# Kernel optimization log

Measured on AMD Instinct MI355X. Metric: run time of the kernel, lower is better.

The kernel has to match this reference:

```python
import jax, jax.numpy as jnp
import numpy as np

B, D, H, T = 4096, 256, 266, 51   # batch, dim, dim+10 hidden, timegrid points
S = T - 1                          # Euler steps
KAPPA, SIGMA = 1.0, 1.0
EPS = 1e-5                         # BatchNorm eps (torch default)


def setup_inputs() -> dict:
    key = jax.random.key(0)
    ks = iter(jax.random.split(key, 16))

    def lin(nin, nout, prefix=()):
        return jax.random.normal(next(ks), prefix + (nin, nout), jnp.float32) / np.float32(np.sqrt(nin))

    inp = {}
    inp["x"] = jax.random.normal(next(ks), (B, D), jnp.float32)
    # per-timestep stacks: Linear+BN params for i_h1, h1_h2, and Linear for h2_o
    inp["W1"] = lin(D, H, (S,));  inp["b1"] = jnp.zeros((S, H));  inp["g1"] = jnp.ones((S, H));  inp["be1"] = jnp.zeros((S, H))
    inp["W2"] = lin(H, H, (S,));  inp["b2"] = jnp.zeros((S, H));  inp["g2"] = jnp.ones((S, H));  inp["be2"] = jnp.zeros((S, H))
    inp["W3"] = lin(H, D, (S,));  inp["b3"] = jnp.zeros((S, D))
    # v0 head: three hiddenLayers (Linear+BN+ReLU), last one width 1
    inp["vW1"] = lin(D, H);  inp["vb1"] = jnp.zeros((H,));  inp["vg1"] = jnp.ones((H,));  inp["vbe1"] = jnp.zeros((H,))
    inp["vW2"] = lin(H, H);  inp["vb2"] = jnp.zeros((H,));  inp["vg2"] = jnp.ones((H,));  inp["vbe2"] = jnp.zeros((H,))
    inp["vW3"] = lin(H, 1);  inp["vb3"] = jnp.zeros((1,));  inp["vg3"] = jnp.ones((1,));  inp["vbe3"] = jnp.zeros((1,))
    # frozen external netAlpha: (dim+1) -> H -> dim MLP
    inp["aW1"] = lin(D + 1, H);  inp["ab1"] = jnp.zeros((H,))
    inp["aW2"] = lin(H, D);      inp["ab2"] = jnp.zeros((D,))
    # law (population mean per step), timegrid, Brownian increments xi
    inp["law"] = jax.random.normal(next(ks), (S, D), jnp.float32) * 0.1
    inp["timegrid"] = jnp.linspace(0.0, 1.0, T, dtype=jnp.float32)
    inp["xi"] = jax.random.normal(next(ks), (S, B, D), jnp.float32)
    return inp


def _bn(h, g, b):
    # BatchNorm1d in training mode: batch stats (biased variance), affine
    mu = h.mean(axis=0)
    var = h.var(axis=0)
    return g * (h - mu) / jnp.sqrt(var + EPS) + b


def _hid(h, W, b, g, be):
    return jax.nn.relu(_bn(h @ W + b, g, be))


def reference(x, W1, b1, g1, be1, W2, b2, g2, be2, W3, b3,
              vW1, vb1, vg1, vbe1, vW2, vb2, vg2, vbe2, vW3, vb3, vg3, vbe3,
              aW1, ab1, aW2, ab2, law, timegrid, xi):
    x0 = x
    # v0 head evaluated on initial x (i == 0 branch)
    v0 = _hid(x0, vW1, vb1, vg1, vbe1)
    v0 = _hid(v0, vW2, vb2, vg2, vbe2)
    v0 = _hid(v0, vW3, vb3, vg3, vbe3)            # [B, 1]

    hs = jnp.diff(timegrid)                        # [S]
    ts = timegrid[:-1]                             # [S]

    def step(carry, inp):
        xc, vc = carry
        (W1i, b1i, g1i, be1i, W2i, b2i, g2i, be2i, W3i, b3i, lawi, ti, hi, xii) = inp
        h1 = _hid(xc, W1i, b1i, g1i, be1i)
        h2 = _hid(h1, W2i, b2i, g2i, be2i)
        grad = h2 @ W3i + b3i                      # [B, D]
        tx = jnp.concatenate([jnp.full((xc.shape[0], 1), ti, xc.dtype), xc], axis=1)
        alpha = jax.nn.relu(tx @ aW1 + ab1) @ aW2 + ab2   # [B, D]
        f = 0.5 * KAPPA * jnp.sum((xc - lawi) ** 2, axis=1) + 0.5 * jnp.sum(alpha ** 2, axis=1)
        sq = SIGMA * jnp.sqrt(hi)
        # diag(grad @ (sigma*sqrt(h)*xi).T) == row-wise dot product
        ito = sq * jnp.sum(grad * xii, axis=1)     # [B]
        vn = vc - (f * hi)[:, None] + ito[:, None]
        xn = xc + alpha * hi + sq * xii
        return (xn, vn), xn

    (xf, v), xs = jax.lax.scan(
        step, (x0, v0),
        (W1, b1, g1, be1, W2, b2, g2, be2, W3, b3, law, ts, hs, xi))
    path = jnp.concatenate([x0[None], xs], axis=0)  # [T, B, D]
    return (v, xf, path)
```

## Files before the change

### kernel.cpp

```cpp
#include <hip/hip_runtime.h>
#include <math.h>

#define B_   4096
#define D_   256
#define H_   266
#define T_   51
#define S_   50
#define HP   320
#define EPSF 1e-5f

typedef __bf16 bf16_t;
typedef __bf16 bf16x8 __attribute__((ext_vector_type(8)));
typedef float  f32x4  __attribute__((ext_vector_type(4)));

#define BM 64
#define BN 64
#define BK 64
#define LDST 72

struct Job {
  const float* A; int lda; int Ka;
  const float* g; const float* be;
  const float* asum; const float* asq;
  int bnA;
  const bf16_t* Wt; int ldw;
  const float* bias;
  const float* trow; const float* tg; int tidx;
  float* C; int ldc; int N; int relu;
  float* ssum; float* ssq;
  int mode;
  const float* xc; const float* xi; const float* law;
  float* xn; float* vacc;
};

__device__ __forceinline__ void load16(const float* p, float* a) {
  const float4* q = (const float4*)p;
  float4 v0 = q[0], v1 = q[1], v2 = q[2], v3 = q[3];
  a[0]=v0.x; a[1]=v0.y; a[2]=v0.z;  a[3]=v0.w;
  a[4]=v1.x; a[5]=v1.y; a[6]=v1.z;  a[7]=v1.w;
  a[8]=v2.x; a[9]=v2.y; a[10]=v2.z; a[11]=v2.w;
  a[12]=v3.x; a[13]=v3.y; a[14]=v3.z; a[15]=v3.w;
}

__global__ __launch_bounds__(256) void mfma_gemm(Job j0, Job j1, Job j2, float invB) {
  Job j = (blockIdx.z == 0) ? j0 : ((blockIdx.z == 1) ? j1 : j2);

  const int r0 = blockIdx.y * BM;
  const int c0 = blockIdx.x * BN;
  if (c0 >= j.N) return;

  __shared__ bf16_t As[BM][LDST];
  __shared__ bf16_t Ws[BN][LDST];
  __shared__ float sc[HP], sh[HP];

  const int tid = threadIdx.x;

  if (j.bnA) {
    for (int k = tid; k < HP; k += 256) {
      if (k < j.Ka) {
        float mu  = j.asum[k] * invB;
        float var = j.asq[k] * invB - mu * mu;
        float s   = j.g[k] * rsqrtf(var + EPSF);
        sc[k] = s; sh[k] = j.be[k] - mu * s;
      } else { sc[k] = 0.f; sh[k] = 0.f; }
    }
  }

  const int wave = tid >> 6;
  const int lane = tid & 63;
  const int wr = (wave >> 1) * 32;
  const int wc = (wave & 1) * 32;
  const int l16 = lane & 15;
  const int lk8 = (lane >> 4) * 8;

  f32x4 acc[2][2] = {};

  const int arow = tid >> 2;
  const int kseg = (tid & 3) * 16;

  const int niter = (j.Ka + BK - 1) / BK;

  const float*  Abase = j.A + (size_t)(r0 + arow) * j.lda + kseg;
  const int     crow  = c0 + arow;
  const bf16_t* Wbase = j.Wt + (size_t)crow * j.ldw + kseg;
  const bool    wok   = crow < j.N;

  float a16[16];
  uint4 wv0 = make_uint4(0,0,0,0), wv1 = make_uint4(0,0,0,0);

  load16(Abase, a16);
  if (wok) {
    const uint4* q = (const uint4*)Wbase;
    wv0 = q[0]; wv1 = q[1];
  }

  for (int it = 0; it < niter; ++it) {
    const int kb = it * BK + kseg;

    __syncthreads();

    bf16x8 p0, p1;
    if (j.bnA) {
      #pragma unroll
      for (int i = 0; i < 8; ++i)
        p0[i] = (bf16_t)fmaxf(fmaf(a16[i], sc[kb + i], sh[kb + i]), 0.f);
      #pragma unroll
      for (int i = 0; i < 8; ++i)
        p1[i] = (bf16_t)fmaxf(fmaf(a16[8 + i], sc[kb + 8 + i], sh[kb + 8 + i]), 0.f);
    } else {
      #pragma unroll
      for (int i = 0; i < 8; ++i) {
        float t = (kb + i < j.Ka) ? a16[i] : 0.f;
        p0[i] = (bf16_t)t;
      }
      #pragma unroll
      for (int i = 0; i < 8; ++i) {
        float t = (kb + 8 + i < j.Ka) ? a16[8 + i] : 0.f;
        p1[i] = (bf16_t)t;
      }
    }
    *(bf16x8*)&As[arow][kseg]     = p0;
    *(bf16x8*)&As[arow][kseg + 8] = p1;
    *(uint4*)&Ws[arow][kseg]      = wv0;
    *(uint4*)&Ws[arow][kseg + 8]  = wv1;

    __syncthreads();

    if (it + 1 < niter) {
      load16(Abase + (size_t)(it + 1) * BK, a16);
      if (wok) {
        const uint4* q = (const uint4*)(Wbase + (size_t)(it + 1) * BK);
        wv0 = q[0]; wv1 = q[1];
      }
    }

    bf16x8 af[2][2], bfr[2][2];
    #pragma unroll
    for (int mi = 0; mi < 2; ++mi)
      #pragma unroll
      for (int kk = 0; kk < 2; ++kk)
        af[mi][kk] = *(const bf16x8*)&As[wr + mi*16 + l16][kk*32 + lk8];
    #pragma unroll
    for (int ni = 0; ni < 2; ++ni)
      #pragma unroll
      for (int kk = 0; kk < 2; ++kk)
        bfr[ni][kk] = *(const bf16x8*)&Ws[wc + ni*16 + l16][kk*32 + lk8];
    #pragma unroll
    for (int kk = 0; kk < 2; ++kk)
      #pragma unroll
      for (int mi = 0; mi < 2; ++mi)
        #pragma unroll
        for (int ni = 0; ni < 2; ++ni)
          acc[mi][ni] = __builtin_amdgcn_mfma_f32_16x16x32_bf16(af[mi][kk], bfr[ni][kk], acc[mi][ni], 0, 0, 0);
  }

  float tb = j.trow ? j.tg[j.tidx] : 0.f;
  float vv[2][2][4];
  #pragma unroll
  for (int ni = 0; ni < 2; ++ni) {
    int col = c0 + wc + ni*16 + l16;
    bool cok = col < j.N;
    float bias = cok ? j.bias[col] : 0.f;
    if (j.trow && cok) bias = fmaf(tb, j.trow[col], bias);
    #pragma unroll
    for (int mi = 0; mi < 2; ++mi)
      #pragma unroll
      for (int r = 0; r < 4; ++r) {
        float v = acc[mi][ni][r] + bias;
        if (j.relu) v = fmaxf(v, 0.f);
        vv[mi][ni][r] = v;
      }
  }

  if (j.mode == 0) {
    #pragma unroll
    for (int ni = 0; ni < 2; ++ni) {
      int col = c0 + wc + ni*16 + l16;
      bool cok = col < j.N;
      float s = 0.f, q = 0.f;
      #pragma unroll
      for (int mi = 0; mi < 2; ++mi)
        #pragma unroll
        for (int r = 0; r < 4; ++r) {
          float v = vv[mi][ni][r];
          int row = r0 + wr + mi*16 + ((lane >> 4) << 2) + r;
          if (cok) j.C[(size_t)row * j.ldc + col] = v;
          s += v; q += v * v;
        }
      if (j.ssum) {
        s += __shfl_xor(s, 16); q += __shfl_xor(q, 16);
        s += __shfl_xor(s, 32); q += __shfl_xor(q, 32);
        if (lane < 16) {
          int col2 = c0 + wc + ni*16 + lane;
          if (col2 < j.N) { atomicAdd(&j.ssum[col2], s); atomicAdd(&j.ssq[col2], q); }
        }
      }
    }
  } else {
    float hi = j.tg[j.tidx + 1] - j.tg[j.tidx];
    float sq = sqrtf(hi);
    #pragma unroll
    for (int mi = 0; mi < 2; ++mi) {
      #pragma unroll
      for (int r = 0; r < 4; ++r) {
        int row = r0 + wr + mi*16 + ((lane >> 4) << 2) + r;
        float part = 0.f;
        #pragma unroll
        for (int ni = 0; ni < 2; ++ni) {
          int col = c0 + wc + ni*16 + l16;
          size_t off = (size_t)row * D_ + col;
          float v = vv[mi][ni][r];
          if (j.mode == 1) {
            float xcv = j.xc[off];
            float xiv = j.xi[off];
            float lw  = j.law[col];
            j.xn[off] = xcv + v * hi + sq * xiv;
            float df = xcv - lw;
            part += df * df + v * v;
          } else {
            part += v * j.xi[off];
          }
        }
        part += __shfl_xor(part, 1); part += __shfl_xor(part, 2);
        part += __shfl_xor(part, 4); part += __shfl_xor(part, 8);
        if (l16 == 0)
          atomicAdd(&j.vacc[row], (j.mode == 1) ? -0.5f * hi * part : sq * part);
      }
    }
  }
}

__global__ __launch_bounds__(256) void wconv(const float* __restrict__ in, bf16_t* __restrict__ out,
                                             int K, int N, int Kp, int total) {
  for (int idx = blockIdx.x * 256 + threadIdx.x; idx < total; idx += gridDim.x * 256) {
    int k = idx % Kp; int rest = idx / Kp; int n = rest % N; int s = rest / N;
    float v = (k < K) ? in[((size_t)s * K + k) * N + n] : 0.f;
    out[idx] = (bf16_t)v;
  }
}

__global__ __launch_bounds__(256) void matvec_bn(const float* __restrict__ A, int lda,
                                                 const float* __restrict__ g, const float* __restrict__ be,
                                                 const float* __restrict__ asum, const float* __restrict__ asq,
                                                 const float* __restrict__ w, const float* __restrict__ bptr,
                                                 float* __restrict__ y, float* ssum, float* ssq,
                                                 int K, float invB) {
  int r = blockIdx.x;
  float acc = 0.f;
  for (int k = threadIdx.x; k < K; k += 256) {
    float mu  = asum[k] * invB;
    float var = asq[k] * invB - mu * mu;
    float s   = g[k] * rsqrtf(var + EPSF);
    float val = fmaxf(fmaf(A[(size_t)r * lda + k], s, be[k] - mu * s), 0.f);
    acc += val * w[k];
  }
  __shared__ float sred[256];
  sred[threadIdx.x] = acc; __syncthreads();
  for (int st = 128; st > 0; st >>= 1) {
    if (threadIdx.x < st) sred[threadIdx.x] += sred[threadIdx.x + st];
    __syncthreads();
  }
  if (threadIdx.x == 0) {
    float v = sred[0] + bptr[0];
    y[r] = v;
    atomicAdd(ssum, v); atomicAdd(ssq, v * v);
  }
}

__global__ __launch_bounds__(256) void v0_fin(const float* __restrict__ y, float* v,
                                              const float* g, const float* be,
                                              const float* ssum, const float* ssq,
                                              int M, float invM) {
  int r = blockIdx.x * blockDim.x + threadIdx.x;
  if (r < M) {
    float mu  = ssum[0] * invM;
    float var = ssq[0] * invM - mu * mu;
    float t = g[0] * (y[r] - mu) * rsqrtf(var + EPSF) + be[0];
    v[r] = fmaxf(t, 0.f);
  }
}

__global__ __launch_bounds__(256) void vadd(float* __restrict__ v, const float* __restrict__ vacc, int M) {
  int r = blockIdx.x * 256 + threadIdx.x;
  if (r < M) v[r] += vacc[r];
}

extern "C" void kernel_launch(void* const* d_in, const int* in_sizes, int n_in,
                              void* d_out, int out_size, void* d_ws, size_t ws_size,
                              hipStream_t stream) {
  const float* x    = (const float*)d_in[0];
  const float* W1   = (const float*)d_in[1];
  const float* b1   = (const float*)d_in[2];
  const float* g1   = (const float*)d_in[3];
  const float* be1  = (const float*)d_in[4];
  const float* W2   = (const float*)d_in[5];
  const float* b2   = (const float*)d_in[6];
  const float* g2   = (const float*)d_in[7];
  const float* be2  = (const float*)d_in[8];
  const float* W3   = (const float*)d_in[9];
  const float* b3   = (const float*)d_in[10];
  const float* vW1  = (const float*)d_in[11];
  const float* vb1  = (const float*)d_in[12];
  const float* vg1  = (const float*)d_in[13];
  const float* vbe1 = (const float*)d_in[14];
  const float* vW2  = (const float*)d_in[15];
  const float* vb2  = (const float*)d_in[16];
  const float* vg2  = (const float*)d_in[17];
  const float* vbe2 = (const float*)d_in[18];
  const float* vW3  = (const float*)d_in[19];
  const float* vb3  = (const float*)d_in[20];
  const float* vg3  = (const float*)d_in[21];
  const float* vbe3 = (const float*)d_in[22];
  const float* aW1  = (const float*)d_in[23];
  const float* ab1  = (const float*)d_in[24];
  const float* aW2  = (const float*)d_in[25];
  const float* ab2  = (const float*)d_in[26];
  const float* law  = (const float*)d_in[27];
  const float* tg   = (const float*)d_in[28];
  const float* xi   = (const float*)d_in[29];

  float* out    = (float*)d_out;
  float* v_out  = out;
  float* xf_out = out + B_;
  float* path   = out + B_ + (size_t)B_ * D_;

  float* ws   = (float*)d_ws;
  float* h1   = ws;
  float* h2   = h1 + (size_t)B_ * HP;
  float* ah   = h2 + (size_t)B_ * HP;
  float* yraw = ah + (size_t)B_ * HP;
  float* stats = yraw + B_;
  const int NSLOT = 2 * S_ + 3;
  float* vacc = stats + (size_t)NSLOT * 2 * HP;

  bf16_t* wbuf = (bf16_t*)(vacc + B_);
  bf16_t* W1t  = wbuf;
  bf16_t* W2t  = W1t + (size_t)S_ * H_ * 256;
  bf16_t* W3t  = W2t + (size_t)S_ * H_ * 320;
  bf16_t* aW1t = W3t + (size_t)S_ * 256 * 320;
  bf16_t* aW2t = aW1t + (size_t)H_ * 256;
  bf16_t* vW1t = aW2t + (size_t)256 * 320;
  bf16_t* vW2t = vW1t + (size_t)H_ * 256;

  hipMemsetAsync(stats, 0, ((size_t)NSLOT * 2 * HP + B_) * sizeof(float), stream);
  hipMemcpyAsync(path, x, (size_t)B_ * D_ * sizeof(float), hipMemcpyDeviceToDevice, stream);

  auto ssum = [&](int s) { return stats + (size_t)s * 2 * HP; };
  auto ssq  = [&](int s) { return stats + (size_t)s * 2 * HP + HP; };

  dim3 blk(256);
  const float invB = 1.0f / (float)B_;
  const int MT   = B_ / BM;
  const int NT_H = (H_ + BN - 1) / BN;
  const int NT_D = D_ / BN;

  wconv<<<dim3(1024), blk, 0, stream>>>(W1,        W1t,  256, H_,  256, S_ * H_ * 256);
  wconv<<<dim3(1024), blk, 0, stream>>>(W2,        W2t,  H_,  H_,  320, S_ * H_ * 320);
  wconv<<<dim3(1024), blk, 0, stream>>>(W3,        W3t,  H_,  256, 320, S_ * 256 * 320);
  wconv<<<dim3(256),  blk, 0, stream>>>(aW1 + H_,  aW1t, 256, H_,  256, H_ * 256);
  wconv<<<dim3(256),  blk, 0, stream>>>(aW2,       aW2t, H_,  256, 320, 256 * 320);
  wconv<<<dim3(256),  blk, 0, stream>>>(vW1,       vW1t, 256, H_,  256, H_ * 256);
  wconv<<<dim3(256),  blk, 0, stream>>>(vW2,       vW2t, H_,  H_,  320, H_ * 320);

  {
    Job jv1 = {x, D_, D_, nullptr, nullptr, nullptr, nullptr, 0,
               vW1t, 256, vb1, nullptr, nullptr, 0,
               h1, HP, H_, 0, ssum(100), ssq(100),
               0, nullptr, nullptr, nullptr, nullptr, nullptr};
    mfma_gemm<<<dim3(NT_H, MT, 1), blk, 0, stream>>>(jv1, jv1, jv1, invB);
    Job jv2 = {h1, HP, H_, vg1, vbe1, ssum(100), ssq(100), 1,
               vW2t, 320, vb2, nullptr, nullptr, 0,
               h2, HP, H_, 0, ssum(101), ssq(101),
               0, nullptr, nullptr, nullptr, nullptr, nullptr};
    mfma_gemm<<<dim3(NT_H, MT, 1), blk, 0, stream>>>(jv2, jv2, jv2, invB);
    matvec_bn<<<dim3(B_), blk, 0, stream>>>(h2, HP, vg2, vbe2, ssum(101), ssq(101),
                                            vW3, vb3, yraw, ssum(102), ssq(102), H_, invB);
    v0_fin<<<dim3(16), blk, 0, stream>>>(yraw, v_out, vg3, vbe3, ssum(102), ssq(102), B_, invB);
  }

  Job jd_prev;
  for (int i = 0; i < S_; ++i) {
    const float* xc   = path + (size_t)i * B_ * D_;
    float* xn         = path + (size_t)(i + 1) * B_ * D_;
    const float* xi_i = xi + (size_t)i * B_ * D_;
    const float* lw_i = law + (size_t)i * D_;

    Job ja = {xc, D_, D_, nullptr, nullptr, nullptr, nullptr, 0,
              W1t + (size_t)i * H_ * 256, 256, b1 + (size_t)i * H_, nullptr, nullptr, 0,
              h1, HP, H_, 0, ssum(2 * i), ssq(2 * i),
              0, nullptr, nullptr, nullptr, nullptr, nullptr};
    Job jb = {xc, D_, D_, nullptr, nullptr, nullptr, nullptr, 0,
              aW1t, 256, ab1, aW1, tg, i,
              ah, HP, H_, 1, nullptr, nullptr,
              0, nullptr, nullptr, nullptr, nullptr, nullptr};
    if (i == 0)
      mfma_gemm<<<dim3(NT_H, MT, 2), blk, 0, stream>>>(ja, jb, jb, invB);
    else
      mfma_gemm<<<dim3(NT_H, MT, 3), blk, 0, stream>>>(ja, jb, jd_prev, invB);

    Job jc = {h1, HP, H_, g1 + (size_t)i * H_, be1 + (size_t)i * H_, ssum(2 * i), ssq(2 * i), 1,
              W2t + (size_t)i * H_ * 320, 320, b2 + (size_t)i * H_, nullptr, nullptr, 0,
              h2, HP, H_, 0, ssum(2 * i + 1), ssq(2 * i + 1),
              0, nullptr, nullptr, nullptr, nullptr, nullptr};
    Job je = {ah, HP, H_, nullptr, nullptr, nullptr, nullptr, 0,
              aW2t, 320, ab2, nullptr, tg, i,
              nullptr, 0, D_, 0, nullptr, nullptr,
              1, xc, xi_i, lw_i, xn, vacc};
    mfma_gemm<<<dim3(NT_H, MT, 2), blk, 0, stream>>>(jc, je, je, invB);

    jd_prev = Job{h2, HP, H_, g2 + (size_t)i * H_, be2 + (size_t)i * H_, ssum(2 * i + 1), ssq(2 * i + 1), 1,
                  W3t + (size_t)i * 256 * 320, 320, b3 + (size_t)i * D_, nullptr, tg, i,
                  nullptr, 0, D_, 0, nullptr, nullptr,
                  2, nullptr, xi_i, nullptr, nullptr, vacc};
  }
  mfma_gemm<<<dim3(NT_D, MT, 1), blk, 0, stream>>>(jd_prev, jd_prev, jd_prev, invB);
  vadd<<<dim3(16), blk, 0, stream>>>(v_out, vacc, B_);

  hipMemcpyAsync(xf_out, path + (size_t)S_ * B_ * D_,
                 (size_t)B_ * D_ * sizeof(float), hipMemcpyDeviceToDevice, stream);
}
```

Before: 2.579 ms.

## Fuse all per-step GEMM launches into one persistent cooperative kernel with grid syncs

Replaces roughly a hundred separate kernel launches (weight conversion, v0 head, and the two GEMM launches per Euler step) with a single persistent cooperative kernel. It walks a host-built table of jobs and phases and uses grid.sync between dependent phases. The v0 third layer now goes through the MFMA tile path using a converted bf16 vW3, the v0 finalize is folded into the first step phase, and the vacc buffer is dropped by accumulating directly into v_out. This removes per-launch overhead and gaps between launches, at the cost of grid-wide barriers, a fixed grid size, a host-to-device table copy on each call, and shared memory now declared in a device function.

```diff
diff --git a/kernel.cpp b/kernel.cpp
--- a/kernel.cpp
+++ b/kernel.cpp
@@ -1,5 +1,11 @@
 #include <hip/hip_runtime.h>
+#include <hip/hip_cooperative_groups.h>
 #include <math.h>
+#include <string.h>
+#include <utility>
+#include <initializer_list>
+
+namespace cg = cooperative_groups;
 
 #define B_   4096
 #define D_   256
@@ -19,6 +25,7 @@
 #define LDST 72
 
 struct Job {
+  int kind;
   const float* A; int lda; int Ka;
   const float* g; const float* be;
   const float* asum; const float* asq;
@@ -33,6 +40,8 @@
   float* xn; float* vacc;
 };
 
+struct Phase { int njobs; int total; int jidx[8]; int tcnt[8]; };
+
 __device__ __forceinline__ void load16(const float* p, float* a) {
   const float4* q = (const float4*)p;
   float4 v0 = q[0], v1 = q[1], v2 = q[2], v3 = q[3];
@@ -42,16 +51,14 @@
   a[12]=v3.x; a[13]=v3.y; a[14]=v3.z; a[15]=v3.w;
 }
 
-__global__ __launch_bounds__(256) void mfma_gemm(Job j0, Job j1, Job j2, float invB) {
-  Job j = (blockIdx.z == 0) ? j0 : ((blockIdx.z == 1) ? j1 : j2);
-
-  const int r0 = blockIdx.y * BM;
-  const int c0 = blockIdx.x * BN;
-  if (c0 >= j.N) return;
-
+__device__ void run_tile(const Job& j, int u, float invB) {
   __shared__ bf16_t As[BM][LDST];
   __shared__ bf16_t Ws[BN][LDST];
   __shared__ float sc[HP], sh[HP];
+
+  const int cN = (j.N + BN - 1) >> 6;
+  const int r0 = (u / cN) * BM;
+  const int c0 = (u % cN) * BN;
 
   const int tid = threadIdx.x;
 
@@ -230,60 +237,45 @@
   }
 }
 
-__global__ __launch_bounds__(256) void wconv(const float* __restrict__ in, bf16_t* __restrict__ out,
-                                             int K, int N, int Kp, int total) {
-  for (int idx = blockIdx.x * 256 + threadIdx.x; idx < total; idx += gridDim.x * 256) {
-    int k = idx % Kp; int rest = idx / Kp; int n = rest % N; int s = rest / N;
-    float v = (k < K) ? in[((size_t)s * K + k) * N + n] : 0.f;
-    out[idx] = (bf16_t)v;
+__global__ __launch_bounds__(256, 3) void scan_all(const Job* __restrict__ jobs,
+                                                   const Phase* __restrict__ phases,
+                                                   int nphase, float invB) {
+  cg::grid_group grid = cg::this_grid();
+  const int tid = threadIdx.x;
+  for (int p = 0; p < nphase; ++p) {
+    const Phase& ph = phases[p];
+    for (int t = blockIdx.x; t < ph.total; t += gridDim.x) {
+      int k = 0, off = t;
+      while (k + 1 < ph.njobs && off >= ph.tcnt[k]) { off -= ph.tcnt[k]; ++k; }
+      const Job& j = jobs[ph.jidx[k]];
+      if (j.kind == 0) {
+        run_tile(j, off, invB);
+      } else if (j.kind == 1) {
+        const int base = off << 16;
+        const int tot  = j.Ka;
+        const int end  = (base + 65536 < tot) ? base + 65536 : tot;
+        const float* in = j.A;
+        bf16_t* outp = (bf16_t*)j.C;
+        const int K = j.lda, N = j.ldc, Kp = j.ldw;
+        for (int idx = base + tid; idx < end; idx += 256) {
+          int kk = idx % Kp; int rest = idx / Kp; int n = rest % N; int s = rest / N;
+          float val = (kk < K) ? in[((size_t)s * K + kk) * N + n] : 0.f;
+          outp[idx] = (bf16_t)val;
+        }
+      } else {
+        int r = off * 256 + tid;
+        float mu  = j.asum[0] * invB;
+        float var = j.asq[0] * invB - mu * mu;
+        float tt  = j.g[0] * (j.A[r] - mu) * rsqrtf(var + EPSF) + j.be[0];
+        j.C[r] = fmaxf(tt, 0.f);
+      }
+    }
+    if (p + 1 < nphase) grid.sync();
   }
 }
 
-__global__ __launch_bounds__(256) void matvec_bn(const float* __restrict__ A, int lda,
-                                                 const float* __restrict__ g, const float* __restrict__ be,
-                                                 const float* __restrict__ asum, const float* __restrict__ asq,
-                                                 const float* __restrict__ w, const float* __restrict__ bptr,
-                                                 float* __restrict__ y, float* ssum, float* ssq,
-                                                 int K, float invB) {
-  int r = blockIdx.x;
-  float acc = 0.f;
-  for (int k = threadIdx.x; k < K; k += 256) {
-    float mu  = asum[k] * invB;
-    float var = asq[k] * invB - mu * mu;
-    float s   = g[k] * rsqrtf(var + EPSF);
-    float val = fmaxf(fmaf(A[(size_t)r * lda + k], s, be[k] - mu * s), 0.f);
-    acc += val * w[k];
-  }
-  __shared__ float sred[256];
-  sred[threadIdx.x] = acc; __syncthreads();
-  for (int st = 128; st > 0; st >>= 1) {
-    if (threadIdx.x < st) sred[threadIdx.x] += sred[threadIdx.x + st];
-    __syncthreads();
-  }
-  if (threadIdx.x == 0) {
-    float v = sred[0] + bptr[0];
-    y[r] = v;
-    atomicAdd(ssum, v); atomicAdd(ssq, v * v);
-  }
-}
-
-__global__ __launch_bounds__(256) void v0_fin(const float* __restrict__ y, float* v,
-                                              const float* g, const float* be,
-                                              const float* ssum, const float* ssq,
-                                              int M, float invM) {
-  int r = blockIdx.x * blockDim.x + threadIdx.x;
-  if (r < M) {
-    float mu  = ssum[0] * invM;
-    float var = ssq[0] * invM - mu * mu;
-    float t = g[0] * (y[r] - mu) * rsqrtf(var + EPSF) + be[0];
-    v[r] = fmaxf(t, 0.f);
-  }
-}
-
-__global__ __launch_bounds__(256) void vadd(float* __restrict__ v, const float* __restrict__ vacc, int M) {
-  int r = blockIdx.x * 256 + threadIdx.x;
-  if (r < M) v[r] += vacc[r];
-}
+struct Tab { Job jobs[272]; Phase phases[112]; };
+static Tab h_tab;
 
 extern "C" void kernel_launch(void* const* d_in, const int* in_sizes, int n_in,
                               void* d_out, int out_size, void* d_ws, size_t ws_size,
@@ -331,9 +323,10 @@
   float* yraw = ah + (size_t)B_ * HP;
   float* stats = yraw + B_;
   const int NSLOT = 2 * S_ + 3;
-  float* vacc = stats + (size_t)NSLOT * 2 * HP;
-
-  bf16_t* wbuf = (bf16_t*)(vacc + B_);
+  float* tabf = stats + (size_t)NSLOT * 2 * HP;
+
+  Tab* d_tab = (Tab*)tabf;
+  bf16_t* wbuf = (bf16_t*)((char*)tabf + ((sizeof(Tab) + 255) & ~(size_t)255));
   bf16_t* W1t  = wbuf;
   bf16_t* W2t  = W1t + (size_t)S_ * H_ * 256;
   bf16_t* W3t  = W2t + (size_t)S_ * H_ * 320;
@@ -341,80 +334,132 @@
   bf16_t* aW2t = aW1t + (size_t)H_ * 256;
   bf16_t* vW1t = aW2t + (size_t)256 * 320;
   bf16_t* vW2t = vW1t + (size_t)H_ * 256;
-
-  hipMemsetAsync(stats, 0, ((size_t)NSLOT * 2 * HP + B_) * sizeof(float), stream);
-  hipMemcpyAsync(path, x, (size_t)B_ * D_ * sizeof(float), hipMemcpyDeviceToDevice, stream);
+  bf16_t* vW3t = vW2t + (size_t)H_ * 320;
 
   auto ssum = [&](int s) { return stats + (size_t)s * 2 * HP; };
   auto ssq  = [&](int s) { return stats + (size_t)s * 2 * HP + HP; };
 
-  dim3 blk(256);
   const float invB = 1.0f / (float)B_;
-  const int MT   = B_ / BM;
-  const int NT_H = (H_ + BN - 1) / BN;
-  const int NT_D = D_ / BN;
-
-  wconv<<<dim3(1024), blk, 0, stream>>>(W1,        W1t,  256, H_,  256, S_ * H_ * 256);
-  wconv<<<dim3(1024), blk, 0, stream>>>(W2,        W2t,  H_,  H_,  320, S_ * H_ * 320);
-  wconv<<<dim3(1024), blk, 0, stream>>>(W3,        W3t,  H_,  256, 320, S_ * 256 * 320);
-  wconv<<<dim3(256),  blk, 0, stream>>>(aW1 + H_,  aW1t, 256, H_,  256, H_ * 256);
-  wconv<<<dim3(256),  blk, 0, stream>>>(aW2,       aW2t, H_,  256, 320, 256 * 320);
-  wconv<<<dim3(256),  blk, 0, stream>>>(vW1,       vW1t, 256, H_,  256, H_ * 256);
-  wconv<<<dim3(256),  blk, 0, stream>>>(vW2,       vW2t, H_,  H_,  320, H_ * 320);
-
+
+  memset(&h_tab, 0, sizeof(h_tab));
+  int nj = 0, np = 0;
+
+  auto wjob = [&](const float* in, bf16_t* outp, int K, int N, int Kp, int total) -> int {
+    Job j{}; j.kind = 1; j.A = in; j.C = (float*)outp;
+    j.lda = K; j.ldc = N; j.ldw = Kp; j.Ka = total;
+    h_tab.jobs[nj] = j; return nj++;
+  };
+  auto gjob = [&](const float* A, int lda, int Ka,
+                  const float* g, const float* be, const float* as, const float* aq, int bnA,
+                  const bf16_t* Wt, int ldw, const float* bias,
+                  const float* trow, int tidx,
+                  float* C, int ldc, int N, int relu,
+                  float* su, float* sq2, int mode,
+                  const float* xc, const float* xii, const float* lw, float* xnp) -> int {
+    Job j{}; j.kind = 0;
+    j.A = A; j.lda = lda; j.Ka = Ka; j.g = g; j.be = be; j.asum = as; j.asq = aq; j.bnA = bnA;
+    j.Wt = Wt; j.ldw = ldw; j.bias = bias; j.trow = trow; j.tg = tg; j.tidx = tidx;
+    j.C = C; j.ldc = ldc; j.N = N; j.relu = relu; j.ssum = su; j.ssq = sq2; j.mode = mode;
+    j.xc = xc; j.xi = xii; j.law = lw; j.xn = xnp; j.vacc = v_out;
+    h_tab.jobs[nj] = j; return nj++;
+  };
+  auto addPhase = [&](std::initializer_list<std::pair<int,int>> items) {
+    Phase p{};
+    for (auto it = items.begin(); it != items.end(); ++it) {
+      p.jidx[p.njobs] = it->first; p.tcnt[p.njobs] = it->second;
+      p.total += it->second; p.njobs++;
+    }
+    h_tab.phases[np++] = p;
+  };
+  auto wt = [](int total) { return (total + 65535) >> 16; };
+
+  int JW[8], WT[8];
+  JW[0] = wjob(W1,       W1t,  256, H_,  256, S_ * H_ * 256);  WT[0] = wt(S_ * H_ * 256);
+  JW[1] = wjob(W2,       W2t,  H_,  H_,  320, S_ * H_ * 320);  WT[1] = wt(S_ * H_ * 320);
+  JW[2] = wjob(W3,       W3t,  H_,  256, 320, S_ * 256 * 320); WT[2] = wt(S_ * 256 * 320);
+  JW[3] = wjob(aW1 + H_, aW1t, 256, H_,  256, H_ * 256);       WT[3] = wt(H_ * 256);
+  JW[4] = wjob(aW2,      aW2t, H_,  256, 320, 256 * 320);      WT[4] = wt(256 * 320);
+  JW[5] = wjob(vW1,      vW1t, 256, H_,  256, H_ * 256);       WT[5] = wt(H_ * 256);
+  JW[6] = wjob(vW2,      vW2t, H_,  H_,  320, H_ * 320);       WT[6] = wt(H_ * 320);
+  JW[7] = wjob(vW3,      vW3t, H_,  1,   320, 320);            WT[7] = wt(320);
+
+  int JV1 = gjob(x, D_, D_, nullptr, nullptr, nullptr, nullptr, 0,
+                 vW1t, 256, vb1, nullptr, 0, h1, HP, H_, 0,
+                 ssum(100), ssq(100), 0, nullptr, nullptr, nullptr, nullptr);
+  int JV2 = gjob(h1, HP, H_, vg1, vbe1, ssum(100), ssq(100), 1,
+                 vW2t, 320, vb2, nullptr, 0, h2, HP, H_, 0,
+                 ssum(101), ssq(101), 0, nullptr, nullptr, nullptr, nullptr);
+  int JV3 = gjob(h2, HP, H_, vg2, vbe2, ssum(101), ssq(101), 1,
+                 vW3t, 320, vb3, nullptr, 0, yraw, 1, 1, 0,
+                 ssum(102), ssq(102), 0, nullptr, nullptr, nullptr, nullptr);
+  int JFIN;
   {
-    Job jv1 = {x, D_, D_, nullptr, nullptr, nullptr, nullptr, 0,
-               vW1t, 256, vb1, nullptr, nullptr, 0,
-               h1, HP, H_, 0, ssum(100), ssq(100),
-               0, nullptr, nullptr, nullptr, nullptr, nullptr};
-    mfma_gemm<<<dim3(NT_H, MT, 1), blk, 0, stream>>>(jv1, jv1, jv1, invB);
-    Job jv2 = {h1, HP, H_, vg1, vbe1, ssum(100), ssq(100), 1,
-               vW2t, 320, vb2, nullptr, nullptr, 0,
-               h2, HP, H_, 0, ssum(101), ssq(101),
-               0, nullptr, nullptr, nullptr, nullptr, nullptr};
-    mfma_gemm<<<dim3(NT_H, MT, 1), blk, 0, stream>>>(jv2, jv2, jv2, invB);
-    matvec_bn<<<dim3(B_), blk, 0, stream>>>(h2, HP, vg2, vbe2, ssum(101), ssq(101),
-                                            vW3, vb3, yraw, ssum(102), ssq(102), H_, invB);
-    v0_fin<<<dim3(16), blk, 0, stream>>>(yraw, v_out, vg3, vbe3, ssum(102), ssq(102), B_, invB);
-  }
-
-  Job jd_prev;
+    Job j{}; j.kind = 2; j.A = yraw; j.g = vg3; j.be = vbe3;
+    j.asum = ssum(102); j.asq = ssq(102); j.C = v_out;
+    h_tab.jobs[nj] = j; JFIN = nj++;
+  }
+
+  int JA[S_], JB[S_], JC[S_], JE[S_], JD[S_];
   for (int i = 0; i < S_; ++i) {
     const float* xc   = path + (size_t)i * B_ * D_;
     float* xn         = path + (size_t)(i + 1) * B_ * D_;
     const float* xi_i = xi + (size_t)i * B_ * D_;
     const float* lw_i = law + (size_t)i * D_;
 
-    Job ja = {xc, D_, D_, nullptr, nullptr, nullptr, nullptr, 0,
-              W1t + (size_t)i * H_ * 256, 256, b1 + (size_t)i * H_, nullptr, nullptr, 0,
-              h1, HP, H_, 0, ssum(2 * i), ssq(2 * i),
-              0, nullptr, nullptr, nullptr, nullptr, nullptr};
-    Job jb = {xc, D_, D_, nullptr, nullptr, nullptr, nullptr, 0,
-              aW1t, 256, ab1, aW1, tg, i,
-              ah, HP, H_, 1, nullptr, nullptr,
-              0, nullptr, nullptr, nullptr, nullptr, nullptr};
-    if (i == 0)
-      mfma_gemm<<<dim3(NT_H, MT, 2), blk, 0, stream>>>(ja, jb, jb, invB);
-    else
-      mfma_gemm<<<dim3(NT_H, MT, 3), blk, 0, stream>>>(ja, jb, jd_prev, invB);
-
-    Job jc = {h1, HP, H_, g1 + (size_t)i * H_, be1 + (size_t)i * H_, ssum(2 * i), ssq(2 * i), 1,
-              W2t + (size_t)i * H_ * 320, 320, b2 + (size_t)i * H_, nullptr, nullptr, 0,
-              h2, HP, H_, 0, ssum(2 * i + 1), ssq(2 * i + 1),
-              0, nullptr, nullptr, nullptr, nullptr, nullptr};
-    Job je = {ah, HP, H_, nullptr, nullptr, nullptr, nullptr, 0,
-              aW2t, 320, ab2, nullptr, tg, i,
-              nullptr, 0, D_, 0, nullptr, nullptr,
-              1, xc, xi_i, lw_i, xn, vacc};
-    mfma_gemm<<<dim3(NT_H, MT, 2), blk, 0, stream>>>(jc, je, je, invB);
-
-    jd_prev = Job{h2, HP, H_, g2 + (size_t)i * H_, be2 + (size_t)i * H_, ssum(2 * i + 1), ssq(2 * i + 1), 1,
-                  W3t + (size_t)i * 256 * 320, 320, b3 + (size_t)i * D_, nullptr, tg, i,
-                  nullptr, 0, D_, 0, nullptr, nullptr,
-                  2, nullptr, xi_i, nullptr, nullptr, vacc};
-  }
-  mfma_gemm<<<dim3(NT_D, MT, 1), blk, 0, stream>>>(jd_prev, jd_prev, jd_prev, invB);
-  vadd<<<dim3(16), blk, 0, stream>>>(v_out, vacc, B_);
+    JA[i] = gjob(xc, D_, D_, nullptr, nullptr, nullptr, nullptr, 0,
+                 W1t + (size_t)i * H_ * 256, 256, b1 + (size_t)i * H_, nullptr, 0,
+                 h1, HP, H_, 0, ssum(2 * i), ssq(2 * i), 0,
+                 nullptr, nullptr, nullptr, nullptr);
+    JB[i] = gjob(xc, D_, D_, nullptr, nullptr, nullptr, nullptr, 0,
+                 aW1t, 256, ab1, aW1, i,
+                 ah, HP, H_, 1, nullptr, nullptr, 0,
+                 nullptr, nullptr, nullptr, nullptr);
+    JC[i] = gjob(h1, HP, H_, g1 + (size_t)i * H_, be1 + (size_t)i * H_, ssum(2 * i), ssq(2 * i), 1,
+                 W2t + (size_t)i * H_ * 320, 320, b2 + (size_t)i * H_, nullptr, 0,
+                 h2, HP, H_, 0, ssum(2 * i + 1), ssq(2 * i + 1), 0,
+                 nullptr, nullptr, nullptr, nullptr);
+    JE[i] = gjob(ah, HP, H_, nullptr, nullptr, nullptr, nullptr, 0,
+                 aW2t, 320, ab2, nullptr, i,
+                 nullptr, 0, D_, 0, nullptr, nullptr, 1,
+                 xc, xi_i, lw_i, xn);
+    JD[i] = gjob(h2, HP, H_, g2 + (size_t)i * H_, be2 + (size_t)i * H_, ssum(2 * i + 1), ssq(2 * i + 1), 1,
+                 W3t + (size_t)i * 256 * 320, 320, b3 + (size_t)i * D_, nullptr, i,
+                 nullptr, 0, D_, 0, nullptr, nullptr, 2,
+                 nullptr, xi_i, nullptr, nullptr);
+  }
+
+  addPhase({{JW[0],WT[0]},{JW[1],WT[1]},{JW[2],WT[2]},{JW[3],WT[3]},
+            {JW[4],WT[4]},{JW[5],WT[5]},{JW[6],WT[6]},{JW[7],WT[7]}});
+  addPhase({{JV1,320}});
+  addPhase({{JV2,320}});
+  addPhase({{JV3,64}});
+  for (int i = 0; i < S_; ++i) {
+    if (i == 0) addPhase({{JA[0],320},{JB[0],320},{JFIN,16}});
+    else        addPhase({{JA[i],320},{JB[i],320},{JD[i-1],256}});
+    addPhase({{JC[i],320},{JE[i],256}});
+  }
+  addPhase({{JD[S_-1],256}});
+
+  hipMemsetAsync(stats, 0, (size_t)NSLOT * 2 * HP * sizeof(float), stream);
+  hipMemcpyAsync(path, x, (size_t)B_ * D_ * sizeof(float), hipMemcpyDeviceToDevice, stream);
+  hipMemcpyAsync(d_tab, &h_tab, sizeof(Tab), hipMemcpyHostToDevice, stream);
+
+  static int s_grid = 0;
+  if (s_grid == 0) {
+    int nb = 0;
+    hipError_t e = hipOccupancyMaxActiveBlocksPerMultiprocessor(&nb, scan_all, 256, 0);
+    if (e != hipSuccess || nb < 1) nb = 1;
+    long g = (long)nb * 256;
+    if (g > 896) g = 896;
+    s_grid = (int)g;
+  }
+
+  const Job* d_jobs = d_tab->jobs;
+  const Phase* d_phases = d_tab->phases;
+  int np_arg = np;
+  float invB_arg = invB;
+  void* kargs[] = { (void*)&d_jobs, (void*)&d_phases, (void*)&np_arg, (void*)&invB_arg };
+  hipLaunchCooperativeKernel(scan_all, dim3(s_grid), dim3(256), kargs, 0, stream);
 
   hipMemcpyAsync(xf_out, path + (size_t)S_ * B_ * D_,
                  (size_t)B_ * D_ * sizeof(float), hipMemcpyDeviceToDevice, stream);
```

New measurement: 8.150 ms. +216.0%, slower.

## Software-pipeline Euler steps across layers in a multi-job persistent launch

Applied to the files above, without the earlier changes.

Replaces the per-step pair of GEMM launches with a generic multi-job kernel that packs tiles from different pipeline stages into one grid. The x-update for step i runs alongside layer 1 of step i, layer 2 of step i-1 and layer 3 of step i-2, so each step needs one launch. The alpha MLP becomes one fused kernel that keeps its hidden activations in shared memory instead of writing them to global. The v0 head's scalar matvec and final BN also become jobs in the first launches. Ping-pong h1/h2 buffers keep the overlapped stages from clobbering each other. The cost is a more complex job dispatch and mixed tile types, which may unbalance the grid.

```diff
diff --git a/kernel.cpp b/kernel.cpp
--- a/kernel.cpp
+++ b/kernel.cpp
@@ -1,5 +1,6 @@
 #include <hip/hip_runtime.h>
 #include <math.h>
+#include <string.h>
 
 #define B_   4096
 #define D_   256
@@ -18,20 +19,20 @@
 #define BK 64
 #define LDST 72
 
+#define FXT 128
+#define LDX 264
+#define LDH 328
+#define SMEM_BYTES 37888
+
 struct Job {
-  const float* A; int lda; int Ka;
-  const float* g; const float* be;
-  const float* asum; const float* asq;
-  int bnA;
-  const bf16_t* Wt; int ldw;
-  const float* bias;
-  const float* trow; const float* tg; int tidx;
-  float* C; int ldc; int N; int relu;
-  float* ssum; float* ssq;
-  int mode;
-  const float* xc; const float* xi; const float* law;
-  float* xn; float* vacc;
+  int kind;
+  int lda, Ka, bnA, ldw, tidx, ldc, N, relu, mode, t0, _pad;
+  const float *A, *g, *be, *asum, *asq, *bias, *bias2, *trow, *tg, *xi, *law;
+  const bf16_t *Wt, *Wt2;
+  float *C, *ssum, *ssq, *xn, *vacc;
 };
+
+struct Pack { Job j[6]; int njobs; float invB; };
 
 __device__ __forceinline__ void load16(const float* p, float* a) {
   const float4* q = (const float4*)p;
@@ -42,17 +43,15 @@
   a[12]=v3.x; a[13]=v3.y; a[14]=v3.z; a[15]=v3.w;
 }
 
-__global__ __launch_bounds__(256) void mfma_gemm(Job j0, Job j1, Job j2, float invB) {
-  Job j = (blockIdx.z == 0) ? j0 : ((blockIdx.z == 1) ? j1 : j2);
-
-  const int r0 = blockIdx.y * BM;
-  const int c0 = blockIdx.x * BN;
-  if (c0 >= j.N) return;
-
-  __shared__ bf16_t As[BM][LDST];
-  __shared__ bf16_t Ws[BN][LDST];
-  __shared__ float sc[HP], sh[HP];
-
+__device__ void run_tile(const Job& j, int u, float invB, char* smem) {
+  bf16_t (*As)[LDST] = (bf16_t(*)[LDST])smem;
+  bf16_t (*Ws)[LDST] = (bf16_t(*)[LDST])(smem + BM*LDST*2);
+  float* sc = (float*)(smem + 2*BM*LDST*2);
+  float* sh = sc + HP;
+
+  const int cN = (j.N + BN - 1) >> 6;
+  const int r0 = (u / cN) * BM;
+  const int c0 = (u % cN) * BN;
   const int tid = threadIdx.x;
 
   if (j.bnA) {
@@ -77,7 +76,6 @@
 
   const int arow = tid >> 2;
   const int kseg = (tid & 3) * 16;
-
   const int niter = (j.Ka + BK - 1) / BK;
 
   const float*  Abase = j.A + (size_t)(r0 + arow) * j.lda + kseg;
@@ -154,14 +152,12 @@
           acc[mi][ni] = __builtin_amdgcn_mfma_f32_16x16x32_bf16(af[mi][kk], bfr[ni][kk], acc[mi][ni], 0, 0, 0);
   }
 
-  float tb = j.trow ? j.tg[j.tidx] : 0.f;
   float vv[2][2][4];
   #pragma unroll
   for (int ni = 0; ni < 2; ++ni) {
     int col = c0 + wc + ni*16 + l16;
     bool cok = col < j.N;
     float bias = cok ? j.bias[col] : 0.f;
-    if (j.trow && cok) bias = fmaf(tb, j.trow[col], bias);
     #pragma unroll
     for (int mi = 0; mi < 2; ++mi)
       #pragma unroll
@@ -208,25 +204,129 @@
         #pragma unroll
         for (int ni = 0; ni < 2; ++ni) {
           int col = c0 + wc + ni*16 + l16;
-          size_t off = (size_t)row * D_ + col;
-          float v = vv[mi][ni][r];
-          if (j.mode == 1) {
-            float xcv = j.xc[off];
-            float xiv = j.xi[off];
-            float lw  = j.law[col];
-            j.xn[off] = xcv + v * hi + sq * xiv;
-            float df = xcv - lw;
-            part += df * df + v * v;
-          } else {
-            part += v * j.xi[off];
-          }
+          part += vv[mi][ni][r] * j.xi[(size_t)row * D_ + col];
         }
         part += __shfl_xor(part, 1); part += __shfl_xor(part, 2);
         part += __shfl_xor(part, 4); part += __shfl_xor(part, 8);
-        if (l16 == 0)
-          atomicAdd(&j.vacc[row], (j.mode == 1) ? -0.5f * hi * part : sq * part);
-      }
-    }
+        if (l16 == 0) atomicAdd(&j.vacc[row], sq * part);
+      }
+    }
+  }
+}
+
+__device__ void run_fused(const Job& j, int u, char* smem) {
+  bf16_t (*Xs)[LDX] = (bf16_t(*)[LDX])smem;
+  bf16_t (*Hs)[LDH] = (bf16_t(*)[LDH])(smem + 32*LDX*2);
+  const int tid = threadIdx.x;
+  const int r0 = u * 32;
+
+  {
+    int row = tid >> 3, seg = (tid & 7) * 32;
+    const float* src = j.A + (size_t)(r0 + row) * D_ + seg;
+    bf16_t* dst = &Xs[row][seg];
+    #pragma unroll
+    for (int c = 0; c < 4; ++c) {
+      float4 v0 = ((const float4*)src)[2*c], v1 = ((const float4*)src)[2*c+1];
+      bf16x8 pk;
+      pk[0]=(bf16_t)v0.x; pk[1]=(bf16_t)v0.y; pk[2]=(bf16_t)v0.z; pk[3]=(bf16_t)v0.w;
+      pk[4]=(bf16_t)v1.x; pk[5]=(bf16_t)v1.y; pk[6]=(bf16_t)v1.z; pk[7]=(bf16_t)v1.w;
+      *(bf16x8*)(dst + c*8) = pk;
+    }
+  }
+  __syncthreads();
+
+  const int wave = tid >> 6, lane = tid & 63;
+  const int l16 = lane & 15, lk8 = (lane >> 4) * 8;
+  const int wc1 = wave * 16;
+  const float t  = j.tg[j.tidx];
+  const float hi = j.tg[j.tidx + 1] - t;
+
+  for (int nc = 0; nc < 5; ++nc) {
+    int col = nc*64 + wc1 + l16;
+    int cr  = (col < H_) ? col : (H_ - 1);
+    const bf16_t* wp = j.Wt + (size_t)cr * 256 + lk8;
+    f32x4 acc[2] = {};
+    #pragma unroll
+    for (int kk = 0; kk < 8; ++kk) {
+      bf16x8 bfv = *(const bf16x8*)(wp + kk*32);
+      #pragma unroll
+      for (int mi = 0; mi < 2; ++mi) {
+        bf16x8 af = *(const bf16x8*)&Xs[mi*16 + l16][kk*32 + lk8];
+        acc[mi] = __builtin_amdgcn_mfma_f32_16x16x32_bf16(af, bfv, acc[mi], 0, 0, 0);
+      }
+    }
+    float bias = (col < H_) ? (j.bias[col] + t * j.trow[col]) : 0.f;
+    #pragma unroll
+    for (int mi = 0; mi < 2; ++mi)
+      #pragma unroll
+      for (int r = 0; r < 4; ++r) {
+        float hv = fmaxf(acc[mi][r] + bias, 0.f);
+        if (col >= H_) hv = 0.f;
+        Hs[mi*16 + ((lane >> 4) << 2) + r][nc*64 + wc1 + l16] = (bf16_t)hv;
+      }
+  }
+  __syncthreads();
+
+  const float sq = sqrtf(hi);
+  float fp[2][4] = {};
+  for (int nc = 0; nc < 4; ++nc) {
+    int col = nc*64 + wc1 + l16;
+    const bf16_t* wp = j.Wt2 + (size_t)col * 320 + lk8;
+    f32x4 acc[2] = {};
+    #pragma unroll
+    for (int kk = 0; kk < 9; ++kk) {
+      bf16x8 bfv = *(const bf16x8*)(wp + kk*32);
+      #pragma unroll
+      for (int mi = 0; mi < 2; ++mi) {
+        bf16x8 af = *(const bf16x8*)&Hs[mi*16 + l16][kk*32 + lk8];
+        acc[mi] = __builtin_amdgcn_mfma_f32_16x16x32_bf16(af, bfv, acc[mi], 0, 0, 0);
+      }
+    }
+    float b2 = j.bias2[col];
+    float lw = j.law[col];
+    #pragma unroll
+    for (int mi = 0; mi < 2; ++mi)
+      #pragma unroll
+      for (int r = 0; r < 4; ++r) {
+        int row = r0 + mi*16 + ((lane >> 4) << 2) + r;
+        size_t off = (size_t)row * D_ + col;
+        float al  = acc[mi][r] + b2;
+        float xcv = j.A[off];
+        float xiv = j.xi[off];
+        j.xn[off] = xcv + al * hi + sq * xiv;
+        float df = xcv - lw;
+        fp[mi][r] += df * df + al * al;
+      }
+  }
+  #pragma unroll
+  for (int mi = 0; mi < 2; ++mi)
+    #pragma unroll
+    for (int r = 0; r < 4; ++r) {
+      float s = fp[mi][r];
+      s += __shfl_xor(s, 1); s += __shfl_xor(s, 2);
+      s += __shfl_xor(s, 4); s += __shfl_xor(s, 8);
+      if (l16 == 0)
+        atomicAdd(&j.vacc[r0 + mi*16 + ((lane >> 4) << 2) + r], -0.5f * hi * s);
+    }
+}
+
+__global__ __launch_bounds__(256) void multi(Pack p) {
+  __shared__ char smem[SMEM_BYTES] __attribute__((aligned(16)));
+  int b = blockIdx.x;
+  int k = p.njobs - 1;
+  while (k > 0 && b < p.j[k].t0) --k;
+  const Job& j = p.j[k];
+  int u = b - j.t0;
+  if (j.kind == 0) {
+    run_tile(j, u, p.invB, smem);
+  } else if (j.kind == 3) {
+    run_fused(j, u, smem);
+  } else {
+    int r = u * 256 + threadIdx.x;
+    float mu  = j.asum[0] * p.invB;
+    float var = j.asq[0] * p.invB - mu * mu;
+    float tt  = j.g[0] * (j.A[r] - mu) * rsqrtf(var + EPSF) + j.be[0];
+    j.C[r] = fmaxf(tt, 0.f);
   }
 }
 
@@ -236,47 +336,6 @@
     int k = idx % Kp; int rest = idx / Kp; int n = rest % N; int s = rest / N;
     float v = (k < K) ? in[((size_t)s * K + k) * N + n] : 0.f;
     out[idx] = (bf16_t)v;
-  }
-}
-
-__global__ __launch_bounds__(256) void matvec_bn(const float* __restrict__ A, int lda,
-                                                 const float* __restrict__ g, const float* __restrict__ be,
-                                                 const float* __restrict__ asum, const float* __restrict__ asq,
-                                                 const float* __restrict__ w, const float* __restrict__ bptr,
-                                                 float* __restrict__ y, float* ssum, float* ssq,
-                                                 int K, float invB) {
-  int r = blockIdx.x;
-  float acc = 0.f;
-  for (int k = threadIdx.x; k < K; k += 256) {
-    float mu  = asum[k] * invB;
-    float var = asq[k] * invB - mu * mu;
-    float s   = g[k] * rsqrtf(var + EPSF);
-    float val = fmaxf(fmaf(A[(size_t)r * lda + k], s, be[k] - mu * s), 0.f);
-    acc += val * w[k];
-  }
-  __shared__ float sred[256];
-  sred[threadIdx.x] = acc; __syncthreads();
-  for (int st = 128; st > 0; st >>= 1) {
-    if (threadIdx.x < st) sred[threadIdx.x] += sred[threadIdx.x + st];
-    __syncthreads();
-  }
-  if (threadIdx.x == 0) {
-    float v = sred[0] + bptr[0];
-    y[r] = v;
-    atomicAdd(ssum, v); atomicAdd(ssq, v * v);
-  }
-}
-
-__global__ __launch_bounds__(256) void v0_fin(const float* __restrict__ y, float* v,
-                                              const float* g, const float* be,
-                                              const float* ssum, const float* ssq,
-                                              int M, float invM) {
-  int r = blockIdx.x * blockDim.x + threadIdx.x;
-  if (r < M) {
-    float mu  = ssum[0] * invM;
-    float var = ssq[0] * invM - mu * mu;
-    float t = g[0] * (y[r] - mu) * rsqrtf(var + EPSF) + be[0];
-    v[r] = fmaxf(t, 0.f);
   }
 }
 
@@ -325,10 +384,13 @@
   float* path   = out + B_ + (size_t)B_ * D_;
 
   float* ws   = (float*)d_ws;
-  float* h1   = ws;
-  float* h2   = h1 + (size_t)B_ * HP;
-  float* ah   = h2 + (size_t)B_ * HP;
-  float* yraw = ah + (size_t)B_ * HP;
+  float* h1a  = ws;
+  float* h1b  = h1a + (size_t)B_ * HP;
+  float* h2a  = h1b + (size_t)B_ * HP;
+  float* h2b  = h2a + (size_t)B_ * HP;
+  float* hv1  = h2b + (size_t)B_ * HP;
+  float* hv2  = hv1 + (size_t)B_ * HP;
+  float* yraw = hv2 + (size_t)B_ * HP;
   float* stats = yraw + B_;
   const int NSLOT = 2 * S_ + 3;
   float* vacc = stats + (size_t)NSLOT * 2 * HP;
@@ -341,79 +403,98 @@
   bf16_t* aW2t = aW1t + (size_t)H_ * 256;
   bf16_t* vW1t = aW2t + (size_t)256 * 320;
   bf16_t* vW2t = vW1t + (size_t)H_ * 256;
+  bf16_t* vW3t = vW2t + (size_t)H_ * 320;
+
+  auto ssum = [&](int s) { return stats + (size_t)s * 2 * HP; };
+  auto ssq  = [&](int s) { return stats + (size_t)s * 2 * HP + HP; };
+
+  const float invB = 1.0f / (float)B_;
 
   hipMemsetAsync(stats, 0, ((size_t)NSLOT * 2 * HP + B_) * sizeof(float), stream);
   hipMemcpyAsync(path, x, (size_t)B_ * D_ * sizeof(float), hipMemcpyDeviceToDevice, stream);
 
-  auto ssum = [&](int s) { return stats + (size_t)s * 2 * HP; };
-  auto ssq  = [&](int s) { return stats + (size_t)s * 2 * HP + HP; };
-
   dim3 blk(256);
-  const float invB = 1.0f / (float)B_;
-  const int MT   = B_ / BM;
-  const int NT_H = (H_ + BN - 1) / BN;
-  const int NT_D = D_ / BN;
-
-  wconv<<<dim3(1024), blk, 0, stream>>>(W1,        W1t,  256, H_,  256, S_ * H_ * 256);
-  wconv<<<dim3(1024), blk, 0, stream>>>(W2,        W2t,  H_,  H_,  320, S_ * H_ * 320);
-  wconv<<<dim3(1024), blk, 0, stream>>>(W3,        W3t,  H_,  256, 320, S_ * 256 * 320);
-  wconv<<<dim3(256),  blk, 0, stream>>>(aW1 + H_,  aW1t, 256, H_,  256, H_ * 256);
-  wconv<<<dim3(256),  blk, 0, stream>>>(aW2,       aW2t, H_,  256, 320, 256 * 320);
-  wconv<<<dim3(256),  blk, 0, stream>>>(vW1,       vW1t, 256, H_,  256, H_ * 256);
-  wconv<<<dim3(256),  blk, 0, stream>>>(vW2,       vW2t, H_,  H_,  320, H_ * 320);
-
-  {
-    Job jv1 = {x, D_, D_, nullptr, nullptr, nullptr, nullptr, 0,
-               vW1t, 256, vb1, nullptr, nullptr, 0,
-               h1, HP, H_, 0, ssum(100), ssq(100),
-               0, nullptr, nullptr, nullptr, nullptr, nullptr};
-    mfma_gemm<<<dim3(NT_H, MT, 1), blk, 0, stream>>>(jv1, jv1, jv1, invB);
-    Job jv2 = {h1, HP, H_, vg1, vbe1, ssum(100), ssq(100), 1,
-               vW2t, 320, vb2, nullptr, nullptr, 0,
-               h2, HP, H_, 0, ssum(101), ssq(101),
-               0, nullptr, nullptr, nullptr, nullptr, nullptr};
-    mfma_gemm<<<dim3(NT_H, MT, 1), blk, 0, stream>>>(jv2, jv2, jv2, invB);
-    matvec_bn<<<dim3(B_), blk, 0, stream>>>(h2, HP, vg2, vbe2, ssum(101), ssq(101),
-                                            vW3, vb3, yraw, ssum(102), ssq(102), H_, invB);
-    v0_fin<<<dim3(16), blk, 0, stream>>>(yraw, v_out, vg3, vbe3, ssum(102), ssq(102), B_, invB);
-  }
-
-  Job jd_prev;
-  for (int i = 0; i < S_; ++i) {
-    const float* xc   = path + (size_t)i * B_ * D_;
-    float* xn         = path + (size_t)(i + 1) * B_ * D_;
-    const float* xi_i = xi + (size_t)i * B_ * D_;
-    const float* lw_i = law + (size_t)i * D_;
-
-    Job ja = {xc, D_, D_, nullptr, nullptr, nullptr, nullptr, 0,
-              W1t + (size_t)i * H_ * 256, 256, b1 + (size_t)i * H_, nullptr, nullptr, 0,
-              h1, HP, H_, 0, ssum(2 * i), ssq(2 * i),
-              0, nullptr, nullptr, nullptr, nullptr, nullptr};
-    Job jb = {xc, D_, D_, nullptr, nullptr, nullptr, nullptr, 0,
-              aW1t, 256, ab1, aW1, tg, i,
-              ah, HP, H_, 1, nullptr, nullptr,
-              0, nullptr, nullptr, nullptr, nullptr, nullptr};
-    if (i == 0)
-      mfma_gemm<<<dim3(NT_H, MT, 2), blk, 0, stream>>>(ja, jb, jb, invB);
-    else
-      mfma_gemm<<<dim3(NT_H, MT, 3), blk, 0, stream>>>(ja, jb, jd_prev, invB);
-
-    Job jc = {h1, HP, H_, g1 + (size_t)i * H_, be1 + (size_t)i * H_, ssum(2 * i), ssq(2 * i), 1,
-              W2t + (size_t)i * H_ * 320, 320, b2 + (size_t)i * H_, nullptr, nullptr, 0,
-              h2, HP, H_, 0, ssum(2 * i + 1), ssq(2 * i + 1),
-              0, nullptr, nullptr, nullptr, nullptr, nullptr};
-    Job je = {ah, HP, H_, nullptr, nullptr, nullptr, nullptr, 0,
-              aW2t, 320, ab2, nullptr, tg, i,
-              nullptr, 0, D_, 0, nullptr, nullptr,
-              1, xc, xi_i, lw_i, xn, vacc};
-    mfma_gemm<<<dim3(NT_H, MT, 2), blk, 0, stream>>>(jc, je, je, invB);
-
-    jd_prev = Job{h2, HP, H_, g2 + (size_t)i * H_, be2 + (size_t)i * H_, ssum(2 * i + 1), ssq(2 * i + 1), 1,
-                  W3t + (size_t)i * 256 * 320, 320, b3 + (size_t)i * D_, nullptr, tg, i,
-                  nullptr, 0, D_, 0, nullptr, nullptr,
-                  2, nullptr, xi_i, nullptr, nullptr, vacc};
-  }
-  mfma_gemm<<<dim3(NT_D, MT, 1), blk, 0, stream>>>(jd_prev, jd_prev, jd_prev, invB);
+  wconv<<<dim3(1024), blk, 0, stream>>>(W1,       W1t,  256, H_,  256, S_ * H_ * 256);
+  wconv<<<dim3(1024), blk, 0, stream>>>(W2,       W2t,  H_,  H_,  320, S_ * H_ * 320);
+  wconv<<<dim3(1024), blk, 0, stream>>>(W3,       W3t,  H_,  256, 320, S_ * 256 * 320);
+  wconv<<<dim3(256),  blk, 0, stream>>>(aW1 + H_, aW1t, 256, H_,  256, H_ * 256);
+  wconv<<<dim3(256),  blk, 0, stream>>>(aW2,      aW2t, H_,  256, 320, 256 * 320);
+  wconv<<<dim3(256),  blk, 0, stream>>>(vW1,      vW1t, 256, H_,  256, H_ * 256);
+  wconv<<<dim3(256),  blk, 0, stream>>>(vW2,      vW2t, H_,  H_,  320, H_ * 320);
+  wconv<<<dim3(2),    blk, 0, stream>>>(vW3,      vW3t, H_,  1,   320, 320);
+
+  auto G = [&](const float* A, int lda, int Ka,
+               const float* g, const float* be, const float* as, const float* aq, int bnA,
+               const bf16_t* Wt, int ldw, const float* bias,
+               float* C, int ldc, int N, int relu,
+               float* su, float* sq2, int mode, int tidx, const float* xii) -> Job {
+    Job j; memset(&j, 0, sizeof(j));
+    j.kind = 0; j.A = A; j.lda = lda; j.Ka = Ka;
+    j.g = g; j.be = be; j.asum = as; j.asq = aq; j.bnA = bnA;
+    j.Wt = Wt; j.ldw = ldw; j.bias = bias;
+    j.C = C; j.ldc = ldc; j.N = N; j.relu = relu;
+    j.ssum = su; j.ssq = sq2; j.mode = mode; j.tidx = tidx;
+    j.tg = tg; j.xi = xii; j.vacc = vacc;
+    return j;
+  };
+  auto tilesOf = [&](const Job& j) -> int {
+    if (j.kind == 0) return (B_ / BM) * ((j.N + BN - 1) >> 6);
+    if (j.kind == 3) return FXT;
+    return 16;
+  };
+  auto launch = [&](Job* js, int n) {
+    Pack p; memset(&p, 0, sizeof(p));
+    int tot = 0;
+    for (int k = 0; k < n; ++k) { p.j[k] = js[k]; p.j[k].t0 = tot; tot += tilesOf(js[k]); }
+    p.njobs = n; p.invB = invB;
+    multi<<<dim3(tot), blk, 0, stream>>>(p);
+  };
+
+  Job jv1 = G(x,   D_, D_, nullptr, nullptr, nullptr, nullptr, 0, vW1t, 256, vb1, hv1, HP, H_, 0, ssum(100), ssq(100), 0, 0, nullptr);
+  Job jv2 = G(hv1, HP, H_, vg1, vbe1, ssum(100), ssq(100), 1,   vW2t, 320, vb2, hv2, HP, H_, 0, ssum(101), ssq(101), 0, 0, nullptr);
+  Job jv3 = G(hv2, HP, H_, vg2, vbe2, ssum(101), ssq(101), 1,   vW3t, 320, vb3, yraw, 1, 1,  0, ssum(102), ssq(102), 0, 0, nullptr);
+  Job jfin; memset(&jfin, 0, sizeof(jfin));
+  jfin.kind = 2; jfin.A = yraw; jfin.g = vg3; jfin.be = vbe3;
+  jfin.asum = ssum(102); jfin.asq = ssq(102); jfin.C = v_out;
+
+  auto mkFX = [&](int i) -> Job {
+    Job j; memset(&j, 0, sizeof(j));
+    j.kind = 3;
+    j.A    = path + (size_t)i * B_ * D_;
+    j.xn   = path + (size_t)(i + 1) * B_ * D_;
+    j.xi   = xi + (size_t)i * B_ * D_;
+    j.law  = law + (size_t)i * D_;
+    j.Wt   = aW1t; j.Wt2 = aW2t;
+    j.bias = ab1;  j.bias2 = ab2; j.trow = aW1;
+    j.tg = tg; j.tidx = i; j.vacc = vacc;
+    return j;
+  };
+  auto mkJA = [&](int i) -> Job {
+    return G(path + (size_t)i * B_ * D_, D_, D_, nullptr, nullptr, nullptr, nullptr, 0,
+             W1t + (size_t)i * H_ * 256, 256, b1 + (size_t)i * H_,
+             (i & 1) ? h1b : h1a, HP, H_, 0, ssum(2*i), ssq(2*i), 0, i, nullptr);
+  };
+  auto mkJC = [&](int i) -> Job {
+    return G((i & 1) ? h1b : h1a, HP, H_, g1 + (size_t)i * H_, be1 + (size_t)i * H_, ssum(2*i), ssq(2*i), 1,
+             W2t + (size_t)i * H_ * 320, 320, b2 + (size_t)i * H_,
+             (i & 1) ? h2b : h2a, HP, H_, 0, ssum(2*i+1), ssq(2*i+1), 0, i, nullptr);
+  };
+  auto mkJD = [&](int i) -> Job {
+    return G((i & 1) ? h2b : h2a, HP, H_, g2 + (size_t)i * H_, be2 + (size_t)i * H_, ssum(2*i+1), ssq(2*i+1), 1,
+             W3t + (size_t)i * 256 * 320, 320, b3 + (size_t)i * D_,
+             nullptr, 0, D_, 0, nullptr, nullptr, 2, i, xi + (size_t)i * B_ * D_);
+  };
+
+  { Job js[1] = { jv1 };                               launch(js, 1); }
+  { Job js[3] = { mkFX(0), mkJA(0), jv2 };             launch(js, 3); }
+  { Job js[4] = { mkFX(1), mkJA(1), mkJC(0), jv3 };    launch(js, 4); }
+  { Job js[5] = { mkFX(2), mkJA(2), mkJC(1), mkJD(0), jfin }; launch(js, 5); }
+  for (int i = 3; i < S_; ++i) {
+    Job js[4] = { mkFX(i), mkJA(i), mkJC(i-1), mkJD(i-2) };
+    launch(js, 4);
+  }
+  { Job js[2] = { mkJC(S_-1), mkJD(S_-2) };            launch(js, 2); }
+  { Job js[1] = { mkJD(S_-1) };                        launch(js, 1); }
   vadd<<<dim3(16), blk, 0, stream>>>(v_out, vacc, B_);
 
   hipMemcpyAsync(xf_out, path + (size_t)S_ * B_ * D_,
```

Measured after the change: 2.539 ms. No clear change (-1.5%).
